# Performance work log

Measured on AMD Instinct MI355X. Metric: run time of the kernel, lower is better.

The kernel has to match this reference:

```python
import jax, jax.numpy as jnp
import numpy as np

N = 100000   # nodes
M = N - 1    # tree edges (child -> parent)
EMB = 512    # embedding_size
ENC = 512    # encoder_size


def setup_inputs() -> dict:
    key = jax.random.key(0)
    ks = jax.random.split(key, 10)
    x = jax.random.normal(ks[0], (N, EMB), jnp.float32)
    h = jax.random.normal(ks[1], (N, ENC), jnp.float32)
    c = jax.random.normal(ks[2], (N, ENC), jnp.float32)
    child_idx = jax.random.randint(ks[3], (M,), 0, N)
    parent_idx = jax.random.randint(ks[4], (M,), 0, N)
    s = 0.05
    W_iou = jax.random.normal(ks[5], (3 * ENC, EMB), jnp.float32) * s
    U_iou = jax.random.normal(ks[6], (3 * ENC, ENC), jnp.float32) * s
    b_iou = jnp.zeros((3 * ENC,), jnp.float32)
    U_f_w = jax.random.normal(ks[7], (ENC, ENC), jnp.float32) * s
    U_f_b = jax.random.normal(ks[8], (ENC,), jnp.float32) * s
    return {"x": x, "h": h, "c": c, "child_idx": child_idx,
            "parent_idx": parent_idx, "W_iou": W_iou, "U_iou": U_iou,
            "b_iou": b_iou, "U_f_w": U_f_w, "U_f_b": U_f_b}


def reference(x, h, c, child_idx, parent_idx, W_iou, U_iou, b_iou, U_f_w, U_f_b):
    n = x.shape[0]
    # message_func: gather child states along edges  [M, ENC]
    h_src = h[child_idx]
    c_src = c[child_idx]
    # reduce_func: forget gate per child, ragged sums over children
    f = jax.nn.sigmoid(h_src @ U_f_w.T + U_f_b)               # [M, ENC]
    h_tilde = jax.ops.segment_sum(h_src, parent_idx, num_segments=n)
    c_red = jax.ops.segment_sum(f * c_src, parent_idx, num_segments=n)
    deg = jax.ops.segment_sum(jnp.ones((h_src.shape[0],), x.dtype),
                              parent_idx, num_segments=n)
    has_child = (deg > 0)[:, None]
    # reduce_func overwrites iou with U_iou(h_tilde) for nodes with children;
    # leaves keep the initial W_iou(x).
    iou = jnp.where(has_child, h_tilde @ U_iou.T, x @ W_iou.T) + b_iou
    i, o, u = jnp.split(iou, 3, axis=1)
    c_new = jax.nn.sigmoid(i) * jnp.tanh(u) + jnp.where(has_child, c_red, 0.0)
    h_new = jax.nn.sigmoid(o) * jnp.tanh(c_new)
    return h_new, c_new
```

## Files before the change

### kernel.cpp

```cpp
#include <hip/hip_runtime.h>
#include <stdint.h>

typedef __bf16 bf16x8 __attribute__((ext_vector_type(8)));
typedef float f32x4 __attribute__((ext_vector_type(4)));
typedef unsigned short ushort8 __attribute__((ext_vector_type(8)));

__device__ __forceinline__ float bf2f(unsigned short u) {
  union { uint32_t i; float f; } v; v.i = ((uint32_t)u) << 16; return v.f;
}
__device__ __forceinline__ unsigned short f2bf(float f) {
  union { uint32_t i; float f; } v; v.f = f;
  uint32_t u = v.i;
  return (unsigned short)((u + 0x7fffu + ((u >> 16) & 1u)) >> 16);
}
__device__ __forceinline__ float sigm(float x) { return 1.0f / (1.0f + __expf(-x)); }
__device__ __forceinline__ float tanh_f(float x) { return 1.0f - 2.0f / (__expf(2.0f * x) + 1.0f); }

__device__ __forceinline__ ushort4 cvt4(float4 a) {
  ushort4 o; o.x = f2bf(a.x); o.y = f2bf(a.y); o.z = f2bf(a.z); o.w = f2bf(a.w); return o;
}

__device__ __forceinline__ int xcd_swz(int bid, int nwg) {
  int q = nwg >> 3, r = nwg & 7;
  int x = bid & 7, idx = bid >> 3;
  return (x < r ? x * (q + 1) : r * (q + 1) + (x - r) * q) + idx;
}

__global__ void k_f2bf(const float* __restrict__ src, unsigned short* __restrict__ dst, long long n8) {
  long long t = (long long)blockIdx.x * blockDim.x + threadIdx.x;
  if (t >= n8) return;
  const float4* s = (const float4*)src + t * 2;
  float4 a = s[0], b = s[1];
  ((ushort4*)dst)[t * 2]     = cvt4(a);
  ((ushort4*)dst)[t * 2 + 1] = cvt4(b);
}

__global__ void k_hist(const int* __restrict__ idx, int* __restrict__ cnt, int M) {
  int e = blockIdx.x * blockDim.x + threadIdx.x;
  if (e < M) atomicAdd(&cnt[idx[e]], 1);
}

__global__ void k_scan1(const int* __restrict__ deg, unsigned long long* __restrict__ ps,
                        unsigned long long* __restrict__ bsum, int Nn) {
  __shared__ unsigned long long tmp[256];
  int t = blockIdx.x * 256 + threadIdx.x;
  int d = (t < Nn) ? deg[t] : 0;
  unsigned long long v = (unsigned long long)(unsigned)d | ((d > 0) ? (1ull << 32) : 0ull);
  tmp[threadIdx.x] = v;
  __syncthreads();
#pragma unroll
  for (int s = 1; s < 256; s <<= 1) {
    unsigned long long a = (threadIdx.x >= (unsigned)s) ? tmp[threadIdx.x - s] : 0;
    __syncthreads();
    tmp[threadIdx.x] += a;
    __syncthreads();
  }
  if (t < Nn) ps[t] = tmp[threadIdx.x] - v;
  if (threadIdx.x == 255) bsum[blockIdx.x] = tmp[255];
}

__global__ void k_scan2(unsigned long long* __restrict__ bsum, int nb,
                        int* __restrict__ meta, int Nn) {
  __shared__ unsigned long long tmp[512];
  int i = threadIdx.x;
  unsigned long long v = (i < nb) ? bsum[i] : 0;
  tmp[i] = v;
  __syncthreads();
#pragma unroll
  for (int s = 1; s < 512; s <<= 1) {
    unsigned long long a = (i >= s) ? tmp[i - s] : 0;
    __syncthreads();
    tmp[i] += a;
    __syncthreads();
  }
  if (i < nb) bsum[i] = tmp[i] - v;
  if (i == 511) {
    int Ni = (int)(tmp[511] >> 32);
    int L0 = ((Ni + 255) >> 8) << 8;
    meta[0] = Ni;
    meta[1] = L0;
    meta[2] = L0 + (Nn - Ni);
  }
}

__global__ void k_scan3(const unsigned long long* __restrict__ ps,
                        const unsigned long long* __restrict__ bsum,
                        const int* __restrict__ meta, const int* __restrict__ deg,
                        int* __restrict__ rs, int* __restrict__ cursor,
                        int* __restrict__ slot, int* __restrict__ nodeof, int Nn) {
  int t = blockIdx.x * 256 + threadIdx.x;
  if (t >= Nn) return;
  unsigned long long p = ps[t] + bsum[blockIdx.x];
  int r  = (int)(p & 0xffffffffull);
  int si = (int)(p >> 32);
  rs[t] = r;
  cursor[t] = r;
  int sl = (deg[t] > 0) ? si : (meta[1] + (t - si));
  slot[t] = sl;
  nodeof[sl] = t;
}

__global__ void k_cscan1(const int* __restrict__ chdeg, int* __restrict__ bs2, int Nn) {
  __shared__ int tmp[256];
  int t = blockIdx.x * 256 + threadIdx.x;
  tmp[threadIdx.x] = (t < Nn && chdeg[t] > 0) ? 1 : 0;
  __syncthreads();
#pragma unroll
  for (int s = 128; s > 0; s >>= 1) {
    if (threadIdx.x < s) tmp[threadIdx.x] += tmp[threadIdx.x + s];
    __syncthreads();
  }
  if (threadIdx.x == 0) bs2[blockIdx.x] = tmp[0];
}

__global__ void k_cscan2(int* __restrict__ bs2, int nb, int* __restrict__ meta) {
  __shared__ int tmp[512];
  int i = threadIdx.x;
  int v = (i < nb) ? bs2[i] : 0;
  tmp[i] = v;
  __syncthreads();
#pragma unroll
  for (int s = 1; s < 512; s <<= 1) {
    int a = (i >= s) ? tmp[i - s] : 0;
    __syncthreads();
    tmp[i] += a;
    __syncthreads();
  }
  if (i < nb) bs2[i] = tmp[i] - v;
  if (i == 511) meta[3] = tmp[511];
}

__global__ void k_cscan3(const int* __restrict__ chdeg, const int* __restrict__ bs2,
                         int* __restrict__ cidx, int* __restrict__ cnodes, int Nn) {
  __shared__ int tmp[256];
  int t = blockIdx.x * 256 + threadIdx.x;
  int v = (t < Nn && chdeg[t] > 0) ? 1 : 0;
  tmp[threadIdx.x] = v;
  __syncthreads();
#pragma unroll
  for (int s = 1; s < 256; s <<= 1) {
    int a = (threadIdx.x >= s) ? tmp[threadIdx.x - s] : 0;
    __syncthreads();
    tmp[threadIdx.x] += a;
    __syncthreads();
  }
  if (t < Nn) {
    int ci = tmp[threadIdx.x] - v + bs2[blockIdx.x];
    cidx[t] = ci;
    if (v) cnodes[ci] = t;
  }
}

__global__ void k_fill(const int* __restrict__ parent, const int* __restrict__ child,
                       int* __restrict__ cursor, int* __restrict__ childlist, int M) {
  int e = blockIdx.x * blockDim.x + threadIdx.x;
  if (e >= M) return;
  int p = parent[e];
  int pos = atomicAdd(&cursor[p], 1);
  childlist[pos] = child[e];
}

__global__ void k_h2bf_compact(const float* __restrict__ h, const int* __restrict__ chdeg,
                               const int* __restrict__ cidx,
                               unsigned short* __restrict__ hbufc, int Nn) {
  long long t = (long long)blockIdx.x * blockDim.x + threadIdx.x;
  int n = (int)(t >> 6);
  if (n >= Nn) return;
  if (chdeg[n] == 0) return;
  int j = ((int)t & 63) * 8;
  const float4* s = (const float4*)(h + (size_t)n * 512 + j);
  size_t d = (size_t)cidx[n] * 512 + j;
  ((ushort4*)(hbufc + d))[0] = cvt4(s[0]);
  ((ushort4*)(hbufc + d))[1] = cvt4(s[1]);
}

__global__ void k_reduce(const unsigned short* __restrict__ hbufc,
                         const unsigned short* __restrict__ fcc, const float* __restrict__ x,
                         const int* __restrict__ rs, const int* __restrict__ childlist,
                         const int* __restrict__ slot, const int* __restrict__ cidx,
                         unsigned short* __restrict__ Zp, unsigned short* __restrict__ credb,
                         int Nn, int M) {
  int p = blockIdx.x * 4 + (threadIdx.x >> 6);
  if (p >= Nn) return;
  int ln = threadIdx.x & 63;
  int j = ln * 8;
  int start = rs[p];
  int end = (p + 1 < Nn) ? rs[p + 1] : M;
  size_t zb = (size_t)slot[p] * 512 + j;
  if (end > start) {
    float hs[8] = {0, 0, 0, 0, 0, 0, 0, 0};
    float cs[8] = {0, 0, 0, 0, 0, 0, 0, 0};
    for (int i = start; i < end; ++i) {
      int ch = childlist[i];
      int ri = cidx[ch];
      size_t cb = (size_t)ri * 512 + j;
      ushort8 hv = *(const ushort8*)(hbufc + cb);
      ushort8 fv = *(const ushort8*)(fcc + cb);
#pragma unroll
      for (int q = 0; q < 8; ++q) {
        hs[q] += bf2f(hv[q]);
        cs[q] += bf2f(fv[q]);
      }
    }
    float4 h0 = {hs[0], hs[1], hs[2], hs[3]}, h1 = {hs[4], hs[5], hs[6], hs[7]};
    float4 c0 = {cs[0], cs[1], cs[2], cs[3]}, c1 = {cs[4], cs[5], cs[6], cs[7]};
    ((ushort4*)(Zp + zb))[0] = cvt4(h0);
    ((ushort4*)(Zp + zb))[1] = cvt4(h1);
    size_t cr = (size_t)p * 512 + j;
    ((ushort4*)(credb + cr))[0] = cvt4(c0);
    ((ushort4*)(credb + cr))[1] = cvt4(c1);
  } else {
    const float4* s = (const float4*)(x + (size_t)p * 512 + j);
    float4 x0 = s[0], x1 = s[1];
    ((ushort4*)(Zp + zb))[0] = cvt4(x0);
    ((ushort4*)(Zp + zb))[1] = cvt4(x1);
  }
}

__global__ __launch_bounds__(512)
void k_gemm_f(const unsigned short* __restrict__ A,
              const unsigned short* __restrict__ Bt,
              const float* __restrict__ bias, const float* __restrict__ cmat,
              const int* __restrict__ meta, const int* __restrict__ cnodes,
              unsigned short* __restrict__ C) {
  __shared__ __align__(16) unsigned short ldsA[2][256 * 32];
  __shared__ __align__(16) unsigned short ldsB[2][128 * 32];
  const int K = 512, ldc = 512;
  const int tid = threadIdx.x;
  const int wv = tid >> 6, ln = tid & 63;
  const int wr = wv >> 1, wc = wv & 1;
  int wg = xcd_swz(blockIdx.x, gridDim.x);
  int rowp = wg >> 2;
  int colp = wg & 3;
  const int row0 = rowp * 256;
  const int col0 = colp * 128;
  const int Mc = meta[3];
  if (row0 >= Mc) return;

  f32x4 acc[4][4] = {};

  auto stage = [&](int buf, int k0) {
#pragma unroll
    for (int rep = 0; rep < 2; ++rep) {
      int cidx2 = rep * 512 + tid;
      int r  = cidx2 >> 2;
      int kc = cidx2 & 3;
      int kp = (kc ^ ((r >> 1) & 3)) * 8;
      int ga = row0 + r; if (ga > Mc - 1) ga = Mc - 1;
      const unsigned short* srcA = A + (size_t)ga * K + k0 + kp;
      __builtin_amdgcn_global_load_lds(
          (const __attribute__((address_space(1))) void*)(void*)srcA,
          (__attribute__((address_space(3))) void*)(&ldsA[buf][(size_t)cidx2 * 8]),
          16, 0, 0);
    }
    {
      int cidx2 = tid;
      int r  = cidx2 >> 2;
      int kc = cidx2 & 3;
      int kp = (kc ^ ((r >> 1) & 3)) * 8;
      const unsigned short* srcB = Bt + (size_t)(col0 + r) * K + k0 + kp;
      __builtin_amdgcn_global_load_lds(
          (const __attribute__((address_space(1))) void*)(void*)srcB,
          (__attribute__((address_space(3))) void*)(&ldsB[buf][(size_t)cidx2 * 8]),
          16, 0, 0);
    }
  };

  const int kcr = ((ln >> 4) ^ ((ln >> 1) & 3)) * 8;
  auto compute = [&](int buf) {
    bf16x8 af[4], bfr[4];
#pragma unroll
    for (int mi = 0; mi < 4; ++mi)
      af[mi] = *(const bf16x8*)(&ldsA[buf][(size_t)(wr * 64 + mi * 16 + (ln & 15)) * 32 + kcr]);
#pragma unroll
    for (int ni = 0; ni < 4; ++ni)
      bfr[ni] = *(const bf16x8*)(&ldsB[buf][(size_t)(wc * 64 + ni * 16 + (ln & 15)) * 32 + kcr]);
#pragma unroll
    for (int mi = 0; mi < 4; ++mi)
#pragma unroll
      for (int ni = 0; ni < 4; ++ni)
        acc[mi][ni] = __builtin_amdgcn_mfma_f32_16x16x32_bf16(bfr[ni], af[mi], acc[mi][ni], 0, 0, 0);
  };

  stage(0, 0);
  int cur = 0;
#pragma unroll
  for (int kt = 0; kt < 15; ++kt) {
    stage(cur ^ 1, (kt + 1) * 32);
    asm volatile("s_waitcnt vmcnt(3)" ::: "memory");
    __builtin_amdgcn_s_barrier();
    compute(cur);
    __builtin_amdgcn_s_barrier();
    cur ^= 1;
  }
  asm volatile("s_waitcnt vmcnt(0)" ::: "memory");
  __builtin_amdgcn_s_barrier();
  compute(cur);

#pragma unroll
  for (int mi = 0; mi < 4; ++mi) {
    int gm = row0 + wr * 64 + mi * 16 + (ln & 15);
    if (gm >= Mc) continue;
    int node = cnodes[gm];
#pragma unroll
    for (int ni = 0; ni < 4; ++ni) {
      int gn = col0 + wc * 64 + ni * 16 + (ln >> 4) * 4;
      float4 bv = *(const float4*)(bias + gn);
      float4 cv = *(const float4*)(cmat + (size_t)node * ldc + gn);
      ushort4 o;
      o.x = f2bf(sigm(acc[mi][ni][0] + bv.x) * cv.x);
      o.y = f2bf(sigm(acc[mi][ni][1] + bv.y) * cv.y);
      o.z = f2bf(sigm(acc[mi][ni][2] + bv.z) * cv.z);
      o.w = f2bf(sigm(acc[mi][ni][3] + bv.w) * cv.w);
      *(ushort4*)(C + (size_t)gm * ldc + gn) = o;
    }
  }
}

__global__ __launch_bounds__(512)
void k_gemm_iou(const unsigned short* __restrict__ Zp,
                const unsigned short* __restrict__ Ub,
                const unsigned short* __restrict__ Wb,
                const float* __restrict__ bias,
                const int* __restrict__ meta,
                const int* __restrict__ nodeof,
                unsigned short* __restrict__ C) {
  __shared__ __align__(16) unsigned short ldsA[2][256 * 32];
  __shared__ __align__(16) unsigned short ldsB[2][128 * 32];
  const int K = 512, ldc = 1536;
  const int tid = threadIdx.x;
  const int wv = tid >> 6, ln = tid & 63;
  const int wr = wv >> 1, wc = wv & 1;
  int wg = xcd_swz(blockIdx.x, gridDim.x);
  int rowp = wg / 12;
  int colp = wg - rowp * 12;
  const int row0 = rowp * 256;
  const int col0 = colp * 128;

  const int Ni = meta[0], L0 = meta[1], lim2 = meta[2];
  const bool internal = row0 < L0;
  const int limit = internal ? Ni : lim2;
  if (row0 >= limit) return;
  const unsigned short* __restrict__ Bt = internal ? Ub : Wb;

  f32x4 acc[4][4] = {};

  auto stage = [&](int buf, int k0) {
#pragma unroll
    for (int rep = 0; rep < 2; ++rep) {
      int cidx2 = rep * 512 + tid;
      int r  = cidx2 >> 2;
      int kc = cidx2 & 3;
      int kp = (kc ^ ((r >> 1) & 3)) * 8;
      int ga = row0 + r; if (ga > limit - 1) ga = limit - 1;
      const unsigned short* srcA = Zp + (size_t)ga * K + k0 + kp;
      __builtin_amdgcn_global_load_lds(
          (const __attribute__((address_space(1))) void*)(void*)srcA,
          (__attribute__((address_space(3))) void*)(&ldsA[buf][(size_t)cidx2 * 8]),
          16, 0, 0);
    }
    {
      int cidx2 = tid;
      int r  = cidx2 >> 2;
      int kc = cidx2 & 3;
      int kp = (kc ^ ((r >> 1) & 3)) * 8;
      const unsigned short* srcB = Bt + (size_t)(col0 + r) * K + k0 + kp;
      __builtin_amdgcn_global_load_lds(
          (const __attribute__((address_space(1))) void*)(void*)srcB,
          (__attribute__((address_space(3))) void*)(&ldsB[buf][(size_t)cidx2 * 8]),
          16, 0, 0);
    }
  };

  const int kcr = ((ln >> 4) ^ ((ln >> 1) & 3)) * 8;
  auto compute = [&](int buf) {
    bf16x8 af[4], bfr[4];
#pragma unroll
    for (int mi = 0; mi < 4; ++mi)
      af[mi] = *(const bf16x8*)(&ldsA[buf][(size_t)(wr * 64 + mi * 16 + (ln & 15)) * 32 + kcr]);
#pragma unroll
    for (int ni = 0; ni < 4; ++ni)
      bfr[ni] = *(const bf16x8*)(&ldsB[buf][(size_t)(wc * 64 + ni * 16 + (ln & 15)) * 32 + kcr]);
#pragma unroll
    for (int mi = 0; mi < 4; ++mi)
#pragma unroll
      for (int ni = 0; ni < 4; ++ni)
        acc[mi][ni] = __builtin_amdgcn_mfma_f32_16x16x32_bf16(bfr[ni], af[mi], acc[mi][ni], 0, 0, 0);
  };

  stage(0, 0);
  int cur = 0;
#pragma unroll
  for (int kt = 0; kt < 15; ++kt) {
    stage(cur ^ 1, (kt + 1) * 32);
    asm volatile("s_waitcnt vmcnt(3)" ::: "memory");
    __builtin_amdgcn_s_barrier();
    compute(cur);
    __builtin_amdgcn_s_barrier();
    cur ^= 1;
  }
  asm volatile("s_waitcnt vmcnt(0)" ::: "memory");
  __builtin_amdgcn_s_barrier();
  compute(cur);

#pragma unroll
  for (int mi = 0; mi < 4; ++mi) {
    int m = row0 + wr * 64 + mi * 16 + (ln & 15);
    if (m >= limit) continue;
    int node = nodeof[m];
    size_t ob = (size_t)node * ldc;
#pragma unroll
    for (int ni = 0; ni < 4; ++ni) {
      int gn = col0 + wc * 64 + ni * 16 + (ln >> 4) * 4;
      float4 bv = *(const float4*)(bias + gn);
      ushort4 o;
      o.x = f2bf(acc[mi][ni][0] + bv.x);
      o.y = f2bf(acc[mi][ni][1] + bv.y);
      o.z = f2bf(acc[mi][ni][2] + bv.z);
      o.w = f2bf(acc[mi][ni][3] + bv.w);
      *(ushort4*)(C + ob + gn) = o;
    }
  }
}

__global__ void k_epilogue(const unsigned short* __restrict__ iou,
                           const unsigned short* __restrict__ credb,
                           const int* __restrict__ deg,
                           float* __restrict__ out, int Nn) {
  long long t = (long long)blockIdx.x * blockDim.x + threadIdx.x;
  int n = (int)(t >> 6);
  if (n >= Nn) return;
  int j = ((int)t & 63) * 8;
  size_t ib = (size_t)n * 1536;
  ushort4 iv0 = *(const ushort4*)(iou + ib + j);
  ushort4 iv1 = *(const ushort4*)(iou + ib + j + 4);
  ushort4 ov0 = *(const ushort4*)(iou + ib + 512 + j);
  ushort4 ov1 = *(const ushort4*)(iou + ib + 512 + j + 4);
  ushort4 uv0 = *(const ushort4*)(iou + ib + 1024 + j);
  ushort4 uv1 = *(const ushort4*)(iou + ib + 1024 + j + 4);

  float carr[8] = {0, 0, 0, 0, 0, 0, 0, 0};
  if (deg[n] > 0) {
    size_t cr = (size_t)n * 512 + j;
    ushort4 c0 = *(const ushort4*)(credb + cr);
    ushort4 c1 = *(const ushort4*)(credb + cr + 4);
    carr[0] = bf2f(c0.x); carr[1] = bf2f(c0.y); carr[2] = bf2f(c0.z); carr[3] = bf2f(c0.w);
    carr[4] = bf2f(c1.x); carr[5] = bf2f(c1.y); carr[6] = bf2f(c1.z); carr[7] = bf2f(c1.w);
  }

  float iarr[8] = {bf2f(iv0.x), bf2f(iv0.y), bf2f(iv0.z), bf2f(iv0.w),
                   bf2f(iv1.x), bf2f(iv1.y), bf2f(iv1.z), bf2f(iv1.w)};
  float oarr[8] = {bf2f(ov0.x), bf2f(ov0.y), bf2f(ov0.z), bf2f(ov0.w),
                   bf2f(ov1.x), bf2f(ov1.y), bf2f(ov1.z), bf2f(ov1.w)};
  float uarr[8] = {bf2f(uv0.x), bf2f(uv0.y), bf2f(uv0.z), bf2f(uv0.w),
                   bf2f(uv1.x), bf2f(uv1.y), bf2f(uv1.z), bf2f(uv1.w)};
  float hn[8], cn[8];
#pragma unroll
  for (int q = 0; q < 8; ++q) {
    float cc = sigm(iarr[q]) * tanh_f(uarr[q]) + carr[q];
    cn[q] = cc;
    hn[q] = sigm(oarr[q]) * tanh_f(cc);
  }
  size_t hb = (size_t)n * 512 + j;
  size_t cb = (size_t)Nn * 512 + hb;
  *(float4*)(out + hb)     = make_float4(hn[0], hn[1], hn[2], hn[3]);
  *(float4*)(out + hb + 4) = make_float4(hn[4], hn[5], hn[6], hn[7]);
  *(float4*)(out + cb)     = make_float4(cn[0], cn[1], cn[2], cn[3]);
  *(float4*)(out + cb + 4) = make_float4(cn[4], cn[5], cn[6], cn[7]);
}

extern "C" void kernel_launch(void* const* d_in, const int* in_sizes, int n_in,
                              void* d_out, int out_size, void* d_ws, size_t ws_size,
                              hipStream_t stream) {
  const float* x     = (const float*)d_in[0];
  const float* h     = (const float*)d_in[1];
  const float* c     = (const float*)d_in[2];
  const int* child   = (const int*)d_in[3];
  const int* parent  = (const int*)d_in[4];
  const float* W_iou = (const float*)d_in[5];
  const float* U_iou = (const float*)d_in[6];
  const float* b_iou = (const float*)d_in[7];
  const float* U_f_w = (const float*)d_in[8];
  const float* U_f_b = (const float*)d_in[9];

  const int Nn = in_sizes[0] / 512;
  const int M  = in_sizes[3];

  float* out = (float*)d_out;

  char* ws = (char*)d_ws;
  auto al = [](size_t v) { return (v + 255) & ~(size_t)255; };
  size_t sz0    = al((size_t)Nn * 1536 * 2);
  size_t offZp  = sz0;
  size_t szZp   = al((size_t)(Nn + 256) * 512 * 2);
  size_t offHb  = offZp + szZp;
  size_t szHb   = al((size_t)Nn * 512 * 2);
  size_t offCr  = offHb + szHb;
  size_t szCr   = al((size_t)Nn * 512 * 2);
  size_t offDeg = offCr + szCr;
  size_t szN4   = al((size_t)Nn * 4);
  size_t offChd = offDeg + szN4;
  size_t offRs  = offChd + szN4;
  size_t offCur = offRs + szN4;
  size_t offSl  = offCur + szN4;
  size_t offNo  = offSl + szN4;
  size_t szNo   = al((size_t)(Nn + 256) * 4);
  size_t offCi  = offNo + szNo;
  size_t offCn  = offCi + szN4;
  size_t offPs  = offCn + szN4;
  size_t szPs   = al((size_t)Nn * 8);
  size_t offCl  = offPs + szPs;
  size_t szCl   = al((size_t)M * 4);
  size_t offBs  = offCl + szCl;
  size_t szBs   = al(512 * 8);
  size_t offBs2 = offBs + szBs;
  size_t szBs2  = al(512 * 4);
  size_t offMt  = offBs2 + szBs2;
  size_t szMt   = 256;
  size_t offWf  = offMt + szMt;
  size_t szWf   = al(512 * 512 * 2);
  size_t offUb  = offWf + szWf;
  size_t szUw   = al((size_t)1536 * 512 * 2);
  size_t offWb  = offUb + szUw;
  size_t needed = offWb + szUw;
  if (ws_size < needed) return;

  unsigned short* fcc   = (unsigned short*)(ws);
  unsigned short* iou   = (unsigned short*)(ws);
  unsigned short* Zp    = (unsigned short*)(ws + offZp);
  unsigned short* hbufc = (unsigned short*)(ws + offHb);
  unsigned short* credb = (unsigned short*)(ws + offCr);
  int*            deg   = (int*)(ws + offDeg);
  int*            chdeg = (int*)(ws + offChd);
  int*            rs    = (int*)(ws + offRs);
  int*            cursor= (int*)(ws + offCur);
  int*            slot  = (int*)(ws + offSl);
  int*            nodeof= (int*)(ws + offNo);
  int*            cidx  = (int*)(ws + offCi);
  int*            cnodes= (int*)(ws + offCn);
  unsigned long long* ps   = (unsigned long long*)(ws + offPs);
  int*            clist = (int*)(ws + offCl);
  unsigned long long* bsum = (unsigned long long*)(ws + offBs);
  int*            bs2   = (int*)(ws + offBs2);
  int*            meta  = (int*)(ws + offMt);
  unsigned short* Wf    = (unsigned short*)(ws + offWf);
  unsigned short* Ub    = (unsigned short*)(ws + offUb);
  unsigned short* Wb    = (unsigned short*)(ws + offWb);

  hipMemsetAsync(deg, 0, 2 * szN4, stream);

  k_f2bf<<<(512 * 512 / 8 + 255) / 256, 256, 0, stream>>>(U_f_w, Wf, 512 * 512 / 8);
  k_f2bf<<<(1536 * 512 / 8 + 255) / 256, 256, 0, stream>>>(U_iou, Ub, 1536 * 512 / 8);
  k_f2bf<<<(1536 * 512 / 8 + 255) / 256, 256, 0, stream>>>(W_iou, Wb, 1536 * 512 / 8);

  int nb1 = (Nn + 255) / 256;
  k_hist<<<(M + 255) / 256, 256, 0, stream>>>(parent, deg, M);
  k_hist<<<(M + 255) / 256, 256, 0, stream>>>(child, chdeg, M);
  k_scan1<<<nb1, 256, 0, stream>>>(deg, ps, bsum, Nn);
  k_scan2<<<1, 512, 0, stream>>>(bsum, nb1, meta, Nn);
  k_scan3<<<nb1, 256, 0, stream>>>(ps, bsum, meta, deg, rs, cursor, slot, nodeof, Nn);
  k_fill<<<(M + 255) / 256, 256, 0, stream>>>(parent, child, cursor, clist, M);
  k_cscan1<<<nb1, 256, 0, stream>>>(chdeg, bs2, Nn);
  k_cscan2<<<1, 512, 0, stream>>>(bs2, nb1, meta);
  k_cscan3<<<nb1, 256, 0, stream>>>(chdeg, bs2, cidx, cnodes, Nn);

  k_h2bf_compact<<<(int)(((long long)Nn * 64 + 255) / 256), 256, 0, stream>>>(h, chdeg, cidx, hbufc, Nn);

  int nbyF = (Nn + 255) / 256;
  k_gemm_f<<<nbyF * 4, 512, 0, stream>>>(hbufc, Wf, U_f_b, c, meta, cnodes, fcc);

  k_reduce<<<(Nn + 3) / 4, 256, 0, stream>>>(hbufc, fcc, x, rs, clist, slot, cidx, Zp, credb, Nn, M);

  int nbyI = (Nn >> 8) + 2;
  k_gemm_iou<<<nbyI * 12, 512, 0, stream>>>(Zp, Ub, Wb, b_iou, meta, nodeof, iou);

  k_epilogue<<<(int)(((long long)Nn * 64 + 255) / 256), 256, 0, stream>>>(iou, credb, deg, out, Nn);
}
```

Measured before the change: 698.0 us.

## Fuse histograms and scans, store compact child indices in child list

The two degree histograms become one kernel. The separate child-compaction scan (three kernels) is folded into the main scan by packing three 21-bit counters into one 64-bit value. The child list now stores compacted row indices directly, which removes one dependent gather per child in the reduce loop, and the next index is prefetched. This cuts four kernel launches and an indirection, but relies on every count fitting in 21 bits.

```diff
diff --git a/kernel.cpp b/kernel.cpp
--- a/kernel.cpp
+++ b/kernel.cpp
@@ -35,17 +35,24 @@
   ((ushort4*)dst)[t * 2 + 1] = cvt4(b);
 }
 
-__global__ void k_hist(const int* __restrict__ idx, int* __restrict__ cnt, int M) {
+__global__ void k_hist2(const int* __restrict__ parent, const int* __restrict__ child,
+                        int* __restrict__ deg, int* __restrict__ chdeg, int M) {
   int e = blockIdx.x * blockDim.x + threadIdx.x;
-  if (e < M) atomicAdd(&cnt[idx[e]], 1);
-}
-
-__global__ void k_scan1(const int* __restrict__ deg, unsigned long long* __restrict__ ps,
+  if (e >= M) return;
+  atomicAdd(&deg[parent[e]], 1);
+  atomicAdd(&chdeg[child[e]], 1);
+}
+
+__global__ void k_scan1(const int* __restrict__ deg, const int* __restrict__ chdeg,
+                        unsigned long long* __restrict__ ps,
                         unsigned long long* __restrict__ bsum, int Nn) {
   __shared__ unsigned long long tmp[256];
   int t = blockIdx.x * 256 + threadIdx.x;
-  int d = (t < Nn) ? deg[t] : 0;
-  unsigned long long v = (unsigned long long)(unsigned)d | ((d > 0) ? (1ull << 32) : 0ull);
+  int d  = (t < Nn) ? deg[t] : 0;
+  int cf = (t < Nn && chdeg[t] > 0) ? 1 : 0;
+  unsigned long long v = (unsigned long long)(unsigned)d
+                       | ((d > 0) ? (1ull << 21) : 0ull)
+                       | ((unsigned long long)cf << 42);
   tmp[threadIdx.x] = v;
   __syncthreads();
 #pragma unroll
@@ -75,89 +82,45 @@
   }
   if (i < nb) bsum[i] = tmp[i] - v;
   if (i == 511) {
-    int Ni = (int)(tmp[511] >> 32);
+    int Ni = (int)((tmp[511] >> 21) & 0x1FFFFF);
     int L0 = ((Ni + 255) >> 8) << 8;
     meta[0] = Ni;
     meta[1] = L0;
     meta[2] = L0 + (Nn - Ni);
+    meta[3] = (int)((tmp[511] >> 42) & 0x1FFFFF);
   }
 }
 
 __global__ void k_scan3(const unsigned long long* __restrict__ ps,
                         const unsigned long long* __restrict__ bsum,
                         const int* __restrict__ meta, const int* __restrict__ deg,
+                        const int* __restrict__ chdeg,
                         int* __restrict__ rs, int* __restrict__ cursor,
-                        int* __restrict__ slot, int* __restrict__ nodeof, int Nn) {
+                        int* __restrict__ slot, int* __restrict__ nodeof,
+                        int* __restrict__ cidx, int* __restrict__ cnodes, int Nn) {
   int t = blockIdx.x * 256 + threadIdx.x;
   if (t >= Nn) return;
   unsigned long long p = ps[t] + bsum[blockIdx.x];
-  int r  = (int)(p & 0xffffffffull);
-  int si = (int)(p >> 32);
+  int r  = (int)(p & 0x1FFFFF);
+  int si = (int)((p >> 21) & 0x1FFFFF);
+  int ci = (int)((p >> 42) & 0x1FFFFF);
   rs[t] = r;
   cursor[t] = r;
   int sl = (deg[t] > 0) ? si : (meta[1] + (t - si));
   slot[t] = sl;
   nodeof[sl] = t;
-}
-
-__global__ void k_cscan1(const int* __restrict__ chdeg, int* __restrict__ bs2, int Nn) {
-  __shared__ int tmp[256];
-  int t = blockIdx.x * 256 + threadIdx.x;
-  tmp[threadIdx.x] = (t < Nn && chdeg[t] > 0) ? 1 : 0;
-  __syncthreads();
-#pragma unroll
-  for (int s = 128; s > 0; s >>= 1) {
-    if (threadIdx.x < s) tmp[threadIdx.x] += tmp[threadIdx.x + s];
-    __syncthreads();
-  }
-  if (threadIdx.x == 0) bs2[blockIdx.x] = tmp[0];
-}
-
-__global__ void k_cscan2(int* __restrict__ bs2, int nb, int* __restrict__ meta) {
-  __shared__ int tmp[512];
-  int i = threadIdx.x;
-  int v = (i < nb) ? bs2[i] : 0;
-  tmp[i] = v;
-  __syncthreads();
-#pragma unroll
-  for (int s = 1; s < 512; s <<= 1) {
-    int a = (i >= s) ? tmp[i - s] : 0;
-    __syncthreads();
-    tmp[i] += a;
-    __syncthreads();
-  }
-  if (i < nb) bs2[i] = tmp[i] - v;
-  if (i == 511) meta[3] = tmp[511];
-}
-
-__global__ void k_cscan3(const int* __restrict__ chdeg, const int* __restrict__ bs2,
-                         int* __restrict__ cidx, int* __restrict__ cnodes, int Nn) {
-  __shared__ int tmp[256];
-  int t = blockIdx.x * 256 + threadIdx.x;
-  int v = (t < Nn && chdeg[t] > 0) ? 1 : 0;
-  tmp[threadIdx.x] = v;
-  __syncthreads();
-#pragma unroll
-  for (int s = 1; s < 256; s <<= 1) {
-    int a = (threadIdx.x >= s) ? tmp[threadIdx.x - s] : 0;
-    __syncthreads();
-    tmp[threadIdx.x] += a;
-    __syncthreads();
-  }
-  if (t < Nn) {
-    int ci = tmp[threadIdx.x] - v + bs2[blockIdx.x];
-    cidx[t] = ci;
-    if (v) cnodes[ci] = t;
-  }
+  cidx[t] = ci;
+  if (chdeg[t] > 0) cnodes[ci] = t;
 }
 
 __global__ void k_fill(const int* __restrict__ parent, const int* __restrict__ child,
+                       const int* __restrict__ cidx,
                        int* __restrict__ cursor, int* __restrict__ childlist, int M) {
   int e = blockIdx.x * blockDim.x + threadIdx.x;
   if (e >= M) return;
   int p = parent[e];
   int pos = atomicAdd(&cursor[p], 1);
-  childlist[pos] = child[e];
+  childlist[pos] = cidx[child[e]];
 }
 
 __global__ void k_h2bf_compact(const float* __restrict__ h, const int* __restrict__ chdeg,
@@ -177,7 +140,7 @@
 __global__ void k_reduce(const unsigned short* __restrict__ hbufc,
                          const unsigned short* __restrict__ fcc, const float* __restrict__ x,
                          const int* __restrict__ rs, const int* __restrict__ childlist,
-                         const int* __restrict__ slot, const int* __restrict__ cidx,
+                         const int* __restrict__ slot,
                          unsigned short* __restrict__ Zp, unsigned short* __restrict__ credb,
                          int Nn, int M) {
   int p = blockIdx.x * 4 + (threadIdx.x >> 6);
@@ -190,9 +153,9 @@
   if (end > start) {
     float hs[8] = {0, 0, 0, 0, 0, 0, 0, 0};
     float cs[8] = {0, 0, 0, 0, 0, 0, 0, 0};
+    int ri = childlist[start];
     for (int i = start; i < end; ++i) {
-      int ch = childlist[i];
-      int ri = cidx[ch];
+      int rin = (i + 1 < end) ? childlist[i + 1] : ri;
       size_t cb = (size_t)ri * 512 + j;
       ushort8 hv = *(const ushort8*)(hbufc + cb);
       ushort8 fv = *(const ushort8*)(fcc + cb);
@@ -201,6 +164,7 @@
         hs[q] += bf2f(hv[q]);
         cs[q] += bf2f(fv[q]);
       }
+      ri = rin;
     }
     float4 h0 = {hs[0], hs[1], hs[2], hs[3]}, h1 = {hs[4], hs[5], hs[6], hs[7]};
     float4 c0 = {cs[0], cs[1], cs[2], cs[3]}, c1 = {cs[4], cs[5], cs[6], cs[7]};
@@ -513,9 +477,7 @@
   size_t szCl   = al((size_t)M * 4);
   size_t offBs  = offCl + szCl;
   size_t szBs   = al(512 * 8);
-  size_t offBs2 = offBs + szBs;
-  size_t szBs2  = al(512 * 4);
-  size_t offMt  = offBs2 + szBs2;
+  size_t offMt  = offBs + szBs;
   size_t szMt   = 256;
   size_t offWf  = offMt + szMt;
   size_t szWf   = al(512 * 512 * 2);
@@ -541,7 +503,6 @@
   unsigned long long* ps   = (unsigned long long*)(ws + offPs);
   int*            clist = (int*)(ws + offCl);
   unsigned long long* bsum = (unsigned long long*)(ws + offBs);
-  int*            bs2   = (int*)(ws + offBs2);
   int*            meta  = (int*)(ws + offMt);
   unsigned short* Wf    = (unsigned short*)(ws + offWf);
   unsigned short* Ub    = (unsigned short*)(ws + offUb);
@@ -554,22 +515,18 @@
   k_f2bf<<<(1536 * 512 / 8 + 255) / 256, 256, 0, stream>>>(W_iou, Wb, 1536 * 512 / 8);
 
   int nb1 = (Nn + 255) / 256;
-  k_hist<<<(M + 255) / 256, 256, 0, stream>>>(parent, deg, M);
-  k_hist<<<(M + 255) / 256, 256, 0, stream>>>(child, chdeg, M);
-  k_scan1<<<nb1, 256, 0, stream>>>(deg, ps, bsum, Nn);
+  k_hist2<<<(M + 255) / 256, 256, 0, stream>>>(parent, child, deg, chdeg, M);
+  k_scan1<<<nb1, 256, 0, stream>>>(deg, chdeg, ps, bsum, Nn);
   k_scan2<<<1, 512, 0, stream>>>(bsum, nb1, meta, Nn);
-  k_scan3<<<nb1, 256, 0, stream>>>(ps, bsum, meta, deg, rs, cursor, slot, nodeof, Nn);
-  k_fill<<<(M + 255) / 256, 256, 0, stream>>>(parent, child, cursor, clist, M);
-  k_cscan1<<<nb1, 256, 0, stream>>>(chdeg, bs2, Nn);
-  k_cscan2<<<1, 512, 0, stream>>>(bs2, nb1, meta);
-  k_cscan3<<<nb1, 256, 0, stream>>>(chdeg, bs2, cidx, cnodes, Nn);
+  k_scan3<<<nb1, 256, 0, stream>>>(ps, bsum, meta, deg, chdeg, rs, cursor, slot, nodeof, cidx, cnodes, Nn);
+  k_fill<<<(M + 255) / 256, 256, 0, stream>>>(parent, child, cidx, cursor, clist, M);
 
   k_h2bf_compact<<<(int)(((long long)Nn * 64 + 255) / 256), 256, 0, stream>>>(h, chdeg, cidx, hbufc, Nn);
 
   int nbyF = (Nn + 255) / 256;
   k_gemm_f<<<nbyF * 4, 512, 0, stream>>>(hbufc, Wf, U_f_b, c, meta, cnodes, fcc);
 
-  k_reduce<<<(Nn + 3) / 4, 256, 0, stream>>>(hbufc, fcc, x, rs, clist, slot, cidx, Zp, credb, Nn, M);
+  k_reduce<<<(Nn + 3) / 4, 256, 0, stream>>>(hbufc, fcc, x, rs, clist, slot, Zp, credb, Nn, M);
 
   int nbyI = (Nn >> 8) + 2;
   k_gemm_iou<<<nbyI * 12, 512, 0, stream>>>(Zp, Ub, Wb, b_iou, meta, nodeof, iou);
```

Result: faster. 683.0 us (-2.1%).
